# Optimization experiments

Measured on AMD Instinct MI355X. Metric: run time of the kernel, lower is better.

Reference implementation:

```python
import jax, jax.numpy as jnp
import numpy as np

# Static problem sizes (uniform T/taus make the ragged edge list static).
B, N, F, T, TAU, S = 8, 384, 64, 192, 192, 5
SINK_SHIFT = T                    # min sink index == T (sinks are the new nodes)
N_SINK, N_SOURCE = TAU, T + TAU - 1


def _edge_indices():
    # tril_indices(T+tau, offset=-1), keep sink >= T  (window=None)
    r, c = np.tril_indices(T + TAU, k=-1)
    m = r >= T
    r, c = r[m], c[m]
    e = r.shape[0]
    batch = np.repeat(np.arange(B), e)
    return (jnp.asarray(batch, jnp.int32),
            jnp.asarray(np.tile(r, B), jnp.int32),
            jnp.asarray(np.tile(c, B), jnp.int32))


def setup_inputs() -> dict:
    key = jax.random.key(0)
    ks = jax.random.split(key, 6)
    batch_idx, sink_idx, source_idx = _edge_indices()
    s1, s2 = 1.0 / np.sqrt(2 * F), 1.0 / np.sqrt(F)
    return {
        "nodes": jax.random.normal(ks[0], (B, N, F), jnp.float32),
        "w1": jax.random.uniform(ks[1], (2 * F, F), jnp.float32, -s1, s1),
        "b1": jnp.zeros((F,), jnp.float32),
        "g1": jnp.ones((F,), jnp.float32),
        "be1": jnp.zeros((F,), jnp.float32),
        "w2": jax.random.uniform(ks[2], (F, F), jnp.float32, -s2, s2),
        "b2": jnp.zeros((F,), jnp.float32),
        "g2": jnp.ones((F,), jnp.float32),
        "be2": jnp.zeros((F,), jnp.float32),
        "w3": jax.random.uniform(ks[3], (F, 1), jnp.float32, -s2, s2),
        "b3": jnp.zeros((1,), jnp.float32),
        "gumbel": jax.random.gumbel(ks[4], (S, B, N_SINK, N_SOURCE), jnp.float32),
        "batch_idx": batch_idx,
        "sink_idx": sink_idx,
        "source_idx": source_idx,
    }


def _ln(x, g, b):
    mu = x.mean(-1, keepdims=True)
    v = ((x - mu) ** 2).mean(-1, keepdims=True)
    return (x - mu) * jax.lax.rsqrt(v + 1e-5) * g + b


def reference(nodes, w1, b1, g1, be1, w2, b2, g2, be2, w3, b3,
              gumbel, batch_idx, sink_idx, source_idx):
    # gather sink/source node pairs: [E, 2F]
    sink = nodes[batch_idx, sink_idx]
    src = nodes[batch_idx, source_idx]
    x = jnp.concatenate([sink, src], axis=-1)
    # edge MLP -> per-edge logit
    h = _ln(jax.nn.relu(x @ w1 + b1), g1, be1)
    h = _ln(jax.nn.relu(h @ w2 + b2), g2, be2)
    logits = (h @ w3 + b3)[:, 0]                     # [E]
    # dense-padded grid filled with finfo.min (as in torch)
    neg = jnp.finfo(jnp.float32).min
    gs = jnp.full((B, N_SINK, N_SOURCE), neg, jnp.float32)
    gs = gs.at[batch_idx, sink_idx - SINK_SHIFT, source_idx].set(logits)
    # hard gumbel-softmax over source dim, S independent samples
    y_soft = jax.nn.softmax(gs[None] + gumbel, axis=-1)      # [S,B,192,383]
    y_hard = jax.nn.one_hot(jnp.argmax(y_soft, -1), N_SOURCE, dtype=y_soft.dtype)
    y = y_soft + jax.lax.stop_gradient(y_hard - y_soft)
    e = y.sum(0)
    # straight-through binarize: forward (e>0), backward identity
    e = e + jax.lax.stop_gradient((e > 0).astype(e.dtype) - e)
    valid = e[batch_idx, sink_idx - SINK_SHIFT, source_idx]
    vals = jnp.where(valid > 0, valid, 0.0)
    # dense equivalent of the sparse COO adjacency (B, N, N)
    return jnp.zeros((B, N, N), jnp.float32).at[batch_idx, sink_idx, source_idx].set(vals)
```

## Files before the change

### kernel.cpp

```cpp
#include <hip/hip_runtime.h>
#include <math.h>
#include <stdint.h>

#define BB 8
#define NN 384
#define FF 64
#define TT 192
#define NSRC 383
#define NSINK 192
#define SS 5
#define NEDGE 441600
#define BN (BB * NN)
#define TILE_E 256
#define NBLKE (NEDGE / TILE_E)
#define OUTV ((BB * NN * NN) / 4)

typedef float f32x2 __attribute__((ext_vector_type(2)));

#if defined(__has_builtin) && __has_builtin(__builtin_elementwise_fma)
#define PKFMA(a, b, c) __builtin_elementwise_fma((a), (b), (c))
#else
#define PKFMA(a, b, c) ((a) * (b) + (c))
#endif

__device__ __forceinline__ float sel8(const float* s, int i) {
  return (i & 4) ? ((i & 2) ? ((i & 1) ? s[7] : s[6]) : ((i & 1) ? s[5] : s[4]))
                 : ((i & 2) ? ((i & 1) ? s[3] : s[2]) : ((i & 1) ? s[1] : s[0]));
}

__global__ __launch_bounds__(64) void prep_all(
    const float* __restrict__ nodes, const float* __restrict__ w1,
    const float* __restrict__ b1,
    const float* __restrict__ w2, const float* __restrict__ b2,
    const float* __restrict__ g1, const float* __restrict__ be1,
    const float* __restrict__ g2, const float* __restrict__ be2,
    const float* __restrict__ w3, const float* __restrict__ b3,
    float* __restrict__ A, float* __restrict__ Bv,
    float* __restrict__ W2kj, float* __restrict__ wcol,
    float* __restrict__ cb, float* __restrict__ gw,
    float* __restrict__ cwsgw) {
  const int blk = blockIdx.x;
  const int k = threadIdx.x;
  if (blk < BN / 4) {
    const int bn0 = blk * 4;
    __shared__ float nd[4][FF];
#pragma unroll
    for (int i = 0; i < 4; ++i) nd[i][k] = nodes[(bn0 + i) * FF + k];
    __syncthreads();
    const float bk = b1[k];
    float a0 = bk, a1 = bk, a2 = bk, a3 = bk;
    float q0 = 0.f, q1 = 0.f, q2 = 0.f, q3 = 0.f;
#pragma unroll 8
    for (int f = 0; f < FF; ++f) {
      const float wt = w1[f * FF + k];
      const float wb = w1[(FF + f) * FF + k];
      const float n0 = nd[0][f], n1 = nd[1][f], n2 = nd[2][f], n3 = nd[3][f];
      a0 = fmaf(n0, wt, a0); a1 = fmaf(n1, wt, a1);
      a2 = fmaf(n2, wt, a2); a3 = fmaf(n3, wt, a3);
      q0 = fmaf(n0, wb, q0); q1 = fmaf(n1, wb, q1);
      q2 = fmaf(n2, wb, q2); q3 = fmaf(n3, wb, q3);
    }
    A[(bn0 + 0) * FF + k] = a0;  Bv[(bn0 + 0) * FF + k] = q0;
    A[(bn0 + 1) * FF + k] = a1;  Bv[(bn0 + 1) * FF + k] = q1;
    A[(bn0 + 2) * FF + k] = a2;  Bv[(bn0 + 2) * FF + k] = q2;
    A[(bn0 + 3) * FF + k] = a3;  Bv[(bn0 + 3) * FF + k] = q3;
  } else {
    const int j = k;
    float cbj = b2[j];
    float wc = 0.f;
    for (int kk = 0; kk < FF; ++kk) {
      const float wraw = w2[kk * FF + j];
      const float w = g1[kk] * wraw;
      W2kj[kk * FF + j] = w;
      wc += w;
      cbj = fmaf(be1[kk], wraw, cbj);
    }
    wcol[j] = wc;
    cb[j] = cbj;
    const float gwj = g2[j] * w3[j];
    gw[j] = gwj;
    __shared__ float sA[FF], sB[FF];
    sA[j] = gwj;
    sB[j] = be2[j] * w3[j];
    __syncthreads();
    if (j == 0) {
      float a = 0.f, bq = 0.f;
      for (int i = 0; i < FF; ++i) { a += sA[i]; bq += sB[i]; }
      cwsgw[0] = b3[0] + bq;
      cwsgw[1] = a;
    }
  }
}

__global__ __launch_bounds__(256, 2) void edge_mlp(
    const float* __restrict__ A, const float* __restrict__ Bv,
    const float* __restrict__ W2kj, const float* __restrict__ wcolg,
    const float* __restrict__ cbg, const float* __restrict__ gwg,
    const float* __restrict__ cwsgw,
    const int* __restrict__ bidx, const int* __restrict__ ridx,
    const int* __restrict__ cidx, float* __restrict__ L,
    float4* __restrict__ outv) {
  __shared__ float Wl[FF][FF];
  __shared__ float X[4][FF][64];

  const int tid = threadIdx.x;
  const int wave = tid >> 6;
  const int lane = tid & 63;

  const int gtid = blockIdx.x * 256 + tid;
  if (gtid < OUTV) outv[gtid] = make_float4(0.f, 0.f, 0.f, 0.f);

  {
    const float4* src = (const float4*)W2kj;
    float4* dst = (float4*)&Wl[0][0];
#pragma unroll
    for (int i = 0; i < 4; ++i) dst[tid + 256 * i] = src[tid + 256 * i];
  }

  const int ge = blockIdx.x * TILE_E + tid;
  const int b = bidx[ge], r = ridx[ge], c = cidx[ge];
  float mu, rstd;
  {
    const float4* pa = (const float4*)(A + (b * NN + r) * FF);
    const float4* pb = (const float4*)(Bv + (b * NN + c) * FF);
    float s = 0.f, q = 0.f;
#pragma unroll
    for (int i = 0; i < 16; ++i) {
      const float4 av = pa[i];
      const float4 bv = pb[i];
      const float x0 = fmaxf(av.x + bv.x, 0.f);
      const float x1 = fmaxf(av.y + bv.y, 0.f);
      const float x2 = fmaxf(av.z + bv.z, 0.f);
      const float x3 = fmaxf(av.w + bv.w, 0.f);
      const int kb = 4 * i;
      X[wave][kb + 0][lane] = x0;
      X[wave][kb + 1][lane] = x1;
      X[wave][kb + 2][lane] = x2;
      X[wave][kb + 3][lane] = x3;
      s += x0; s += x1; s += x2; s += x3;
      q = fmaf(x0, x0, q); q = fmaf(x1, x1, q);
      q = fmaf(x2, x2, q); q = fmaf(x3, x3, q);
    }
    mu = s * (1.f / FF);
    rstd = 1.f / sqrtf(q * (1.f / FF) - mu * mu + 1e-5f);
  }

  __syncthreads();

  const int joct = lane & 7;
  const int eg3 = lane >> 3;
  f32x2 t2[8][4];
#pragma unroll
  for (int ei = 0; ei < 8; ++ei)
#pragma unroll
    for (int p = 0; p < 4; ++p) t2[ei][p] = (f32x2){0.f, 0.f};

  const float* xrow = &X[wave][0][8 * eg3];
  const float* wrow = &Wl[0][8 * joct];
#pragma unroll 4
  for (int k = 0; k < FF; ++k) {
    const float4 xA = *(const float4*)xrow;
    const float4 xB = *(const float4*)(xrow + 4);
    xrow += 64;
    const float4 wA = *(const float4*)wrow;
    const float4 wB = *(const float4*)(wrow + 4);
    wrow += 64;
    f32x2 w01; w01.x = wA.x; w01.y = wA.y;
    f32x2 w23; w23.x = wA.z; w23.y = wA.w;
    f32x2 w45; w45.x = wB.x; w45.y = wB.y;
    f32x2 w67; w67.x = wB.z; w67.y = wB.w;
    const float xe[8] = {xA.x, xA.y, xA.z, xA.w, xB.x, xB.y, xB.z, xB.w};
#pragma unroll
    for (int ei = 0; ei < 8; ++ei) {
      f32x2 xb; xb.x = xe[ei]; xb.y = xe[ei];
      t2[ei][0] = PKFMA(xb, w01, t2[ei][0]);
      t2[ei][1] = PKFMA(xb, w23, t2[ei][1]);
      t2[ei][2] = PKFMA(xb, w45, t2[ei][2]);
      t2[ei][3] = PKFMA(xb, w67, t2[ei][3]);
    }
  }

  float wc[8], cbv[8], gwv[8];
  *(float4*)&wc[0] = *(const float4*)(wcolg + 8 * joct);
  *(float4*)&wc[4] = *(const float4*)(wcolg + 8 * joct + 4);
  *(float4*)&cbv[0] = *(const float4*)(cbg + 8 * joct);
  *(float4*)&cbv[4] = *(const float4*)(cbg + 8 * joct + 4);
  *(float4*)&gwv[0] = *(const float4*)(gwg + 8 * joct);
  *(float4*)&gwv[4] = *(const float4*)(gwg + 8 * joct + 4);
  const float cw = cwsgw[0], sgw = cwsgw[1];

  const int base8 = lane & 56;
  float s1[8], s2[8], s3[8];
#pragma unroll
  for (int ei = 0; ei < 8; ++ei) {
    const float m = __shfl(mu, base8 + ei, 64);
    const float rs = __shfl(rstd, base8 + ei, 64);
    float a1 = 0.f, a2 = 0.f, a3 = 0.f;
#pragma unroll
    for (int jj = 0; jj < 8; ++jj) {
      const float tv = (jj & 1) ? t2[ei][jj >> 1].y : t2[ei][jj >> 1].x;
      const float pre = fmaf(rs, fmaf(-m, wc[jj], tv), cbv[jj]);
      const float tr = fmaxf(pre, 0.f);
      a1 += tr;
      a2 = fmaf(tr, tr, a2);
      a3 = fmaf(tr, gwv[jj], a3);
    }
    s1[ei] = a1; s2[ei] = a2; s3[ei] = a3;
  }
#pragma unroll
  for (int off = 1; off <= 4; off <<= 1) {
#pragma unroll
    for (int ei = 0; ei < 8; ++ei) {
      s1[ei] += __shfl_xor(s1[ei], off, 64);
      s2[ei] += __shfl_xor(s2[ei], off, 64);
      s3[ei] += __shfl_xor(s3[ei], off, 64);
    }
  }
  const float S1 = sel8(s1, joct);
  const float S2 = sel8(s2, joct);
  const float S3 = sel8(s3, joct);
  const float mu2 = S1 * (1.f / FF);
  const float var2 = S2 * (1.f / FF) - mu2 * mu2;
  const float rstd2 = 1.f / sqrtf(var2 + 1e-5f);
  const float logit = fmaf(rstd2, fmaf(-mu2, sgw, S3), cw);
  L[(b * NSINK + (r - TT)) * NSRC + c] = logit;
}

__global__ __launch_bounds__(256) void argmax_scatter(
    const float* __restrict__ L, const float* __restrict__ gum,
    float* __restrict__ out) {
  const int task = blockIdx.x * 4 + (threadIdx.x >> 6);
  const int lane = threadIdx.x & 63;
  const int row = task % NSINK;
  const int sb = task / NSINK;
  const int b = sb & 7;
  const int r = row + TT;

  const float* __restrict__ lrow = L + (b * NSINK + row) * NSRC;
  const float* __restrict__ grow = gum + task * NSRC;

  float bv = -INFINITY;
  int bi = 0;
  for (int c = lane; c < r; c += 64) {
    const float v = lrow[c] + grow[c];
    if (v > bv) { bv = v; bi = c; }
  }
#pragma unroll
  for (int off = 32; off > 0; off >>= 1) {
    const float ov = __shfl_xor(bv, off, 64);
    const int oi = __shfl_xor(bi, off, 64);
    if (ov > bv || (ov == bv && oi < bi)) { bv = ov; bi = oi; }
  }
  if (lane == 0) out[(b * NN + r) * NN + bi] = 1.0f;
}

extern "C" void kernel_launch(void* const* d_in, const int* in_sizes, int n_in,
                              void* d_out, int out_size, void* d_ws, size_t ws_size,
                              hipStream_t stream) {
  const float* nodes = (const float*)d_in[0];
  const float* w1 = (const float*)d_in[1];
  const float* b1 = (const float*)d_in[2];
  const float* g1 = (const float*)d_in[3];
  const float* be1 = (const float*)d_in[4];
  const float* w2 = (const float*)d_in[5];
  const float* b2 = (const float*)d_in[6];
  const float* g2 = (const float*)d_in[7];
  const float* be2 = (const float*)d_in[8];
  const float* w3 = (const float*)d_in[9];
  const float* b3 = (const float*)d_in[10];
  const float* gum = (const float*)d_in[11];
  const int* bidx = (const int*)d_in[12];
  const int* ridx = (const int*)d_in[13];
  const int* cidx = (const int*)d_in[14];
  float* out = (float*)d_out;

  float* ws = (float*)d_ws;
  float* A = ws;
  float* Bv = A + BN * FF;
  float* W2kj = Bv + BN * FF;
  float* wcol = W2kj + FF * FF;
  float* cb = wcol + FF;
  float* gw = cb + FF;
  float* cwsgw = gw + FF;
  float* L = ws + 397520;
  (void)ws_size; (void)n_in; (void)in_sizes; (void)out_size;

  hipLaunchKernelGGL(prep_all, dim3(BN / 4 + 1), dim3(64), 0, stream,
                     nodes, w1, b1, w2, b2, g1, be1, g2, be2, w3, b3,
                     A, Bv, W2kj, wcol, cb, gw, cwsgw);
  hipLaunchKernelGGL(edge_mlp, dim3(NBLKE), dim3(256), 0, stream,
                     A, Bv, W2kj, wcol, cb, gw, cwsgw, bidx, ridx, cidx, L,
                     (float4*)out);
  hipLaunchKernelGGL(argmax_scatter, dim3((SS * BB * NSINK) / 4), dim3(256), 0, stream,
                     L, gum, out);
}
```

Measured before the change: 153.6 us.

## Split edge MLP work across thread pairs and output halves to cut registers

```diff
diff --git a/kernel.cpp b/kernel.cpp
--- a/kernel.cpp
+++ b/kernel.cpp
@@ -11,7 +11,7 @@
 #define SS 5
 #define NEDGE 441600
 #define BN (BB * NN)
-#define TILE_E 256
+#define TILE_E 128
 #define NBLKE (NEDGE / TILE_E)
 #define OUTV ((BB * NN * NN) / 4)
 
@@ -92,7 +92,7 @@
   }
 }
 
-__global__ __launch_bounds__(256, 2) void edge_mlp(
+__global__ __launch_bounds__(256, 3) void edge_mlp(
     const float* __restrict__ A, const float* __restrict__ Bv,
     const float* __restrict__ W2kj, const float* __restrict__ wcolg,
     const float* __restrict__ cbg, const float* __restrict__ gwg,
@@ -101,11 +101,11 @@
     const int* __restrict__ cidx, float* __restrict__ L,
     float4* __restrict__ outv) {
   __shared__ float Wl[FF][FF];
-  __shared__ float X[4][FF][64];
+  __shared__ float X[2][FF][64];
+  __shared__ float St[TILE_E][2];
+  __shared__ float Sp[2][TILE_E][4];
 
   const int tid = threadIdx.x;
-  const int wave = tid >> 6;
-  const int lane = tid & 63;
 
   const int gtid = blockIdx.x * 256 + tid;
   if (gtid < OUTV) outv[gtid] = make_float4(0.f, 0.f, 0.f, 0.f);
@@ -117,93 +117,104 @@
     for (int i = 0; i < 4; ++i) dst[tid + 256 * i] = src[tid + 256 * i];
   }
 
-  const int ge = blockIdx.x * TILE_E + tid;
+  const int el = tid >> 1;
+  const int kh = tid & 1;
+  const int ge = blockIdx.x * TILE_E + el;
   const int b = bidx[ge], r = ridx[ge], c = cidx[ge];
-  float mu, rstd;
   {
-    const float4* pa = (const float4*)(A + (b * NN + r) * FF);
-    const float4* pb = (const float4*)(Bv + (b * NN + c) * FF);
+    const float4* pa = (const float4*)(A + (b * NN + r) * FF + kh * 32);
+    const float4* pb = (const float4*)(Bv + (b * NN + c) * FF + kh * 32);
+    const int slab1 = el >> 6, e64 = el & 63;
     float s = 0.f, q = 0.f;
 #pragma unroll
-    for (int i = 0; i < 16; ++i) {
+    for (int i = 0; i < 8; ++i) {
       const float4 av = pa[i];
       const float4 bv = pb[i];
       const float x0 = fmaxf(av.x + bv.x, 0.f);
       const float x1 = fmaxf(av.y + bv.y, 0.f);
       const float x2 = fmaxf(av.z + bv.z, 0.f);
       const float x3 = fmaxf(av.w + bv.w, 0.f);
-      const int kb = 4 * i;
-      X[wave][kb + 0][lane] = x0;
-      X[wave][kb + 1][lane] = x1;
-      X[wave][kb + 2][lane] = x2;
-      X[wave][kb + 3][lane] = x3;
+      const int kb = kh * 32 + 4 * i;
+      X[slab1][kb + 0][e64] = x0;
+      X[slab1][kb + 1][e64] = x1;
+      X[slab1][kb + 2][e64] = x2;
+      X[slab1][kb + 3][e64] = x3;
       s += x0; s += x1; s += x2; s += x3;
       q = fmaf(x0, x0, q); q = fmaf(x1, x1, q);
       q = fmaf(x2, x2, q); q = fmaf(x3, x3, q);
     }
-    mu = s * (1.f / FF);
-    rstd = 1.f / sqrtf(q * (1.f / FF) - mu * mu + 1e-5f);
+    s += __shfl_xor(s, 1, 64);
+    q += __shfl_xor(q, 1, 64);
+    const float mu = s * (1.f / FF);
+    const float rstd = 1.f / sqrtf(q * (1.f / FF) - mu * mu + 1e-5f);
+    St[el][kh] = kh ? rstd : mu;
   }
 
   __syncthreads();
 
-  const int joct = lane & 7;
-  const int eg3 = lane >> 3;
-  f32x2 t2[8][4];
-#pragma unroll
-  for (int ei = 0; ei < 8; ++ei)
-#pragma unroll
-    for (int p = 0; p < 4; ++p) t2[ei][p] = (f32x2){0.f, 0.f};
-
-  const float* xrow = &X[wave][0][8 * eg3];
-  const float* wrow = &Wl[0][8 * joct];
+  const int wave = tid >> 6;
+  const int lane = tid & 63;
+  const int slab = wave >> 1;
+  const int jh = wave & 1;
+  const int ep4 = lane >> 3;
+  const int j4 = lane & 7;
+  const int j0 = 32 * jh + 4 * j4;
+
+  f32x2 t2[4][4];
+#pragma unroll
+  for (int p = 0; p < 4; ++p)
+#pragma unroll
+    for (int j = 0; j < 4; ++j) t2[p][j] = (f32x2){0.f, 0.f};
+
+  const float* xrow = &X[slab][0][8 * ep4];
+  const float* wrow = &Wl[0][j0];
 #pragma unroll 4
   for (int k = 0; k < FF; ++k) {
     const float4 xA = *(const float4*)xrow;
     const float4 xB = *(const float4*)(xrow + 4);
     xrow += 64;
-    const float4 wA = *(const float4*)wrow;
-    const float4 wB = *(const float4*)(wrow + 4);
+    const float4 wv = *(const float4*)wrow;
     wrow += 64;
-    f32x2 w01; w01.x = wA.x; w01.y = wA.y;
-    f32x2 w23; w23.x = wA.z; w23.y = wA.w;
-    f32x2 w45; w45.x = wB.x; w45.y = wB.y;
-    f32x2 w67; w67.x = wB.z; w67.y = wB.w;
-    const float xe[8] = {xA.x, xA.y, xA.z, xA.w, xB.x, xB.y, xB.z, xB.w};
-#pragma unroll
-    for (int ei = 0; ei < 8; ++ei) {
-      f32x2 xb; xb.x = xe[ei]; xb.y = xe[ei];
-      t2[ei][0] = PKFMA(xb, w01, t2[ei][0]);
-      t2[ei][1] = PKFMA(xb, w23, t2[ei][1]);
-      t2[ei][2] = PKFMA(xb, w45, t2[ei][2]);
-      t2[ei][3] = PKFMA(xb, w67, t2[ei][3]);
-    }
-  }
-
-  float wc[8], cbv[8], gwv[8];
-  *(float4*)&wc[0] = *(const float4*)(wcolg + 8 * joct);
-  *(float4*)&wc[4] = *(const float4*)(wcolg + 8 * joct + 4);
-  *(float4*)&cbv[0] = *(const float4*)(cbg + 8 * joct);
-  *(float4*)&cbv[4] = *(const float4*)(cbg + 8 * joct + 4);
-  *(float4*)&gwv[0] = *(const float4*)(gwg + 8 * joct);
-  *(float4*)&gwv[4] = *(const float4*)(gwg + 8 * joct + 4);
-  const float cw = cwsgw[0], sgw = cwsgw[1];
-
-  const int base8 = lane & 56;
+    f32x2 xp[4];
+    xp[0].x = xA.x; xp[0].y = xA.y;
+    xp[1].x = xA.z; xp[1].y = xA.w;
+    xp[2].x = xB.x; xp[2].y = xB.y;
+    xp[3].x = xB.z; xp[3].y = xB.w;
+    f32x2 ws[4];
+    ws[0].x = wv.x; ws[0].y = wv.x;
+    ws[1].x = wv.y; ws[1].y = wv.y;
+    ws[2].x = wv.z; ws[2].y = wv.z;
+    ws[3].x = wv.w; ws[3].y = wv.w;
+#pragma unroll
+    for (int p = 0; p < 4; ++p)
+#pragma unroll
+      for (int j = 0; j < 4; ++j)
+        t2[p][j] = PKFMA(xp[p], ws[j], t2[p][j]);
+  }
+
+  const float4 wc4 = *(const float4*)(wcolg + j0);
+  const float4 cb4 = *(const float4*)(cbg + j0);
+  const float4 gw4 = *(const float4*)(gwg + j0);
+  const float wc[4] = {wc4.x, wc4.y, wc4.z, wc4.w};
+  const float cbv[4] = {cb4.x, cb4.y, cb4.z, cb4.w};
+  const float gwv[4] = {gw4.x, gw4.y, gw4.z, gw4.w};
+
   float s1[8], s2[8], s3[8];
 #pragma unroll
   for (int ei = 0; ei < 8; ++ei) {
-    const float m = __shfl(mu, base8 + ei, 64);
-    const float rs = __shfl(rstd, base8 + ei, 64);
+    const int eloc = slab * 64 + 8 * ep4 + ei;
+    const float2 st = *(const float2*)&St[eloc][0];
+    const float m = st.x, rs = st.y;
+    const int p = ei >> 1;
     float a1 = 0.f, a2 = 0.f, a3 = 0.f;
 #pragma unroll
-    for (int jj = 0; jj < 8; ++jj) {
-      const float tv = (jj & 1) ? t2[ei][jj >> 1].y : t2[ei][jj >> 1].x;
-      const float pre = fmaf(rs, fmaf(-m, wc[jj], tv), cbv[jj]);
+    for (int j = 0; j < 4; ++j) {
+      const float tv = (ei & 1) ? t2[p][j].y : t2[p][j].x;
+      const float pre = fmaf(rs, fmaf(-m, wc[j], tv), cbv[j]);
       const float tr = fmaxf(pre, 0.f);
       a1 += tr;
       a2 = fmaf(tr, tr, a2);
-      a3 = fmaf(tr, gwv[jj], a3);
+      a3 = fmaf(tr, gwv[j], a3);
     }
     s1[ei] = a1; s2[ei] = a2; s3[ei] = a3;
   }
@@ -216,14 +227,26 @@
       s3[ei] += __shfl_xor(s3[ei], off, 64);
     }
   }
-  const float S1 = sel8(s1, joct);
-  const float S2 = sel8(s2, joct);
-  const float S3 = sel8(s3, joct);
-  const float mu2 = S1 * (1.f / FF);
-  const float var2 = S2 * (1.f / FF) - mu2 * mu2;
-  const float rstd2 = 1.f / sqrtf(var2 + 1e-5f);
-  const float logit = fmaf(rstd2, fmaf(-mu2, sgw, S3), cw);
-  L[(b * NSINK + (r - TT)) * NSRC + c] = logit;
+  {
+    const int eloc = slab * 64 + 8 * ep4 + j4;
+    Sp[jh][eloc][0] = sel8(s1, j4);
+    Sp[jh][eloc][1] = sel8(s2, j4);
+    Sp[jh][eloc][2] = sel8(s3, j4);
+  }
+
+  __syncthreads();
+
+  if (kh == 0) {
+    const float S1 = Sp[0][el][0] + Sp[1][el][0];
+    const float S2 = Sp[0][el][1] + Sp[1][el][1];
+    const float S3 = Sp[0][el][2] + Sp[1][el][2];
+    const float cw = cwsgw[0], sgw = cwsgw[1];
+    const float mu2 = S1 * (1.f / FF);
+    const float var2 = S2 * (1.f / FF) - mu2 * mu2;
+    const float rstd2 = 1.f / sqrtf(var2 + 1e-5f);
+    const float logit = fmaf(rstd2, fmaf(-mu2, sgw, S3), cw);
+    L[(b * NSINK + (r - TT)) * NSRC + c] = logit;
+  }
 }
 
 __global__ __launch_bounds__(256) void argmax_scatter(
```

New measurement: 167.2 us. 8.8% more time.
